# Kernel optimization log

Measured on AMD Instinct MI355X. Metric: run time of the kernel, lower is better.

The kernel has to match this reference:

```python
import jax, jax.numpy as jnp
import numpy as np

B, S, D = 16, 4096, 64
N_HASHES, BUCKET_SIZE = 8, 64
TOKEN_SELF_ATTN_VALUE = -50000.0


def setup_inputs() -> dict:
    key = jax.random.key(0)
    k1, k2, k3 = jax.random.split(key, 3)
    qk = jax.random.normal(k1, (B, S, D), jnp.float32)
    v = jax.random.normal(k2, (B, S, D), jnp.float32)
    # random rotations for LSH hashing: (batch, dim, n_hashes, n_buckets//2)
    rotations = jax.random.normal(k3, (B, D, N_HASHES, (S // BUCKET_SIZE) // 2), jnp.float32)
    return {"qk": qk, "v": v, "rotations": rotations}


def _look_one_back(x):
    # concat each chunk with the previous chunk (wrapping): (b, c, n, ...) -> (b, c, 2n, ...)
    return jnp.concatenate([x, jnp.roll(x, 1, axis=1)], axis=2)


def _lsh_attention(qk, v, rotations):
    b, s, d = qk.shape
    n_buckets = s // BUCKET_SIZE
    # --- hash vectors (rehash_each_round=True path) ---
    rotated = jnp.einsum('btf,bfhi->bhti', qk, rotations)          # (b, h, s, nb/2)
    rotated = jnp.concatenate([rotated, -rotated], axis=-1)        # (b, h, s, nb)
    buckets = jnp.argmax(rotated, axis=-1)                          # (b, h, s)
    offsets = (jnp.arange(N_HASHES) * n_buckets)[None, :, None]
    buckets = (buckets + offsets).reshape(b, -1)                    # (b, h*s)
    # --- stable bucket sort of tokens ---
    ticker = jnp.arange(N_HASHES * s)[None, :]
    buckets_and_t = s * buckets + ticker % s
    sticker = jnp.argsort(buckets_and_t, axis=-1)                   # sorted order
    undo_sort = jnp.argsort(sticker, axis=-1)
    st = sticker % s                                                # original token index
    sqk = jnp.take_along_axis(qk, st[..., None], axis=1)            # (b, h*s, d)
    sv = jnp.take_along_axis(v, st[..., None], axis=1)
    chunk_size = N_HASHES * n_buckets
    bq_t = st.reshape(b, chunk_size, -1)                            # (b, c, n)
    bqk = sqk.reshape(b, chunk_size, -1, d)                         # (b, c, n, d)
    bv = sv.reshape(b, chunk_size, -1, d)
    # shared-QK: keys are L2-normalized queries
    norm = jnp.linalg.norm(bqk, axis=-1, keepdims=True)
    bk = bqk / jnp.maximum(norm, 1e-12)
    bk = _look_one_back(bk)                                         # (b, c, 2n, d)
    bvl = _look_one_back(bv)
    bkv_t = _look_one_back(bq_t)                                    # (b, c, 2n)
    dots = jnp.einsum('bhie,bhje->bhij', bqk, bk) * (d ** -0.5)     # (b, c, n, 2n)
    # mask self-attention (token attends to itself only as last resort)
    self_mask = bq_t[:, :, :, None] == bkv_t[:, :, None, :]
    dots = jnp.where(self_mask, TOKEN_SELF_ATTN_VALUE, dots)
    # stable softmax per chunk; keep logsumexp for cross-round combination
    lse = jax.nn.logsumexp(dots, axis=-1, keepdims=True)            # (b, c, n, 1)
    p = jnp.exp(dots - lse)
    bo = jnp.einsum('buij,buje->buie', p, bvl)                      # (b, c, n, d)
    so = bo.reshape(b, -1, d)                                       # (b, h*s, d)
    slogits = lse.reshape(b, -1)                                    # (b, h*s)
    # undo the sort
    o = jnp.take_along_axis(so, undo_sort[..., None], axis=1)
    logits = jnp.take_along_axis(slogits, undo_sort, axis=1)
    o = o.reshape(b, N_HASHES, s, d)
    logits = logits.reshape(b, N_HASHES, s, 1)
    # combine hash rounds weighted by softmax over per-round logsumexp
    probs = jnp.exp(logits - jax.nn.logsumexp(logits, axis=1, keepdims=True))
    return jnp.sum(o * probs, axis=1)                               # (b, s, d)


def reference(qk, v, rotations):
    return _lsh_attention(qk, v, rotations)
```

## Files before the change

### kernel.cpp

```cpp
#include <hip/hip_runtime.h>
#include <math.h>

#define NB_B 16
#define NB_S 4096
#define NB_D 64
#define NB_H 8

#define KSTR 72
#define PSTR 136
#define VSTR 72

typedef _Float16 half_t;
typedef __attribute__((ext_vector_type(2))) _Float16 half2t;
typedef __attribute__((ext_vector_type(4))) _Float16 half4;
typedef __attribute__((ext_vector_type(8))) _Float16 half8;
typedef __attribute__((ext_vector_type(4))) float floatx4;

__global__ __launch_bounds__(256) void prep_kernel(const float* __restrict__ qk,
                                                   const float* __restrict__ v,
                                                   half_t* __restrict__ khat,
                                                   half_t* __restrict__ vh,
                                                   float* __restrict__ norm) {
  int g = blockIdx.x * 256 + threadIdx.x;
  float4 qv = ((const float4*)qk)[g];
  float4 vv = ((const float4*)v)[g];
  float ss = qv.x * qv.x + qv.y * qv.y + qv.z * qv.z + qv.w * qv.w;
  for (int off = 1; off < 16; off <<= 1) ss += __shfl_xor(ss, off);
  float nr = fmaxf(sqrtf(ss), 1e-12f);
  float sc = 1.0f / nr;
  half4 hk = {(half_t)(qv.x * sc), (half_t)(qv.y * sc), (half_t)(qv.z * sc),
              (half_t)(qv.w * sc)};
  half4 hv = {(half_t)vv.x, (half_t)vv.y, (half_t)vv.z, (half_t)vv.w};
  ((half4*)khat)[g] = hk;
  ((half4*)vh)[g] = hv;
  if ((threadIdx.x & 15) == 0) norm[g >> 4] = nr;
}

__global__ __launch_bounds__(256) void hash_kernel(const float* __restrict__ qk,
                                                   const float* __restrict__ rot,
                                                   int* __restrict__ bkt) {
  __shared__ float rotS[64 * 32];
  int tid = threadIdx.x;
  int blk = blockIdx.x;
  int tile = blk & 15, bh = blk >> 4;
  int h = bh & 7, b = bh >> 3;
  int t = (tile << 8) + tid;

  for (int i = tid; i < 2048; i += 256) {
    int f = i >> 5, ii = i & 31;
    rotS[i] = rot[(((size_t)b * 64 + f) * 8 + h) * 32 + ii];
  }
  __syncthreads();

  const float4* qrow = (const float4*)(qk + (((size_t)b << 12) + t) * 64);
  float qreg[64];
#pragma unroll
  for (int j = 0; j < 16; j++) *(float4*)(qreg + 4 * j) = qrow[j];

  float acc[32];
#pragma unroll
  for (int i = 0; i < 32; i++) acc[i] = 0.f;

#pragma unroll
  for (int f = 0; f < 64; f++) {
    float qf = qreg[f];
#pragma unroll
    for (int i4 = 0; i4 < 8; i4++) {
      float4 w = *(const float4*)(rotS + f * 32 + i4 * 4);
      acc[i4 * 4 + 0] = __fadd_rn(acc[i4 * 4 + 0], __fmul_rn(qf, w.x));
      acc[i4 * 4 + 1] = __fadd_rn(acc[i4 * 4 + 1], __fmul_rn(qf, w.y));
      acc[i4 * 4 + 2] = __fadd_rn(acc[i4 * 4 + 2], __fmul_rn(qf, w.z));
      acc[i4 * 4 + 3] = __fadd_rn(acc[i4 * 4 + 3], __fmul_rn(qf, w.w));
    }
  }

  float b1 = acc[0];
  int i1 = 0;
#pragma unroll
  for (int i = 1; i < 32; i++)
    if (acc[i] > b1) { b1 = acc[i]; i1 = i; }
#pragma unroll
  for (int i = 0; i < 32; i++) {
    float x = -acc[i];
    if (x > b1) { b1 = x; i1 = 32 + i; }
  }
  bkt[(((size_t)(b * 8 + h)) << 12) + t] = i1;
}

__global__ __launch_bounds__(256) void sort_kernel(const int* __restrict__ bkt,
                                                   int* __restrict__ st) {
  __shared__ int lb[4096];
  __shared__ int hist[4096];
  __shared__ int cumoff[64];
  int tid = threadIdx.x;
  int b = blockIdx.x >> 3, h = blockIdx.x & 7;
  const int* gb = bkt + (((size_t)(b * 8 + h)) << 12);
  for (int t = tid; t < 4096; t += 256) lb[t] = gb[t];
  for (int i = tid; i < 4096; i += 256) hist[i] = 0;
  __syncthreads();
  for (int t = tid; t < 4096; t += 256) atomicAdd(&hist[((t >> 6) << 6) | lb[t]], 1);
  __syncthreads();
  if (tid < 64) {
    int run = 0;
    for (int cc = 0; cc < 64; cc++) {
      int x = hist[(cc << 6) | tid];
      hist[(cc << 6) | tid] = run;
      run += x;
    }
    int s = run;
    for (int off = 1; off < 64; off <<= 1) {
      int u = __shfl_up(s, off);
      if (tid >= off) s += u;
    }
    cumoff[tid] = s - run;
  }
  __syncthreads();
  int lane = tid & 63;
  for (int p = 0; p < 16; p++) {
    int t = (p << 8) + tid;
    int vb = lb[t];
    unsigned long long m = 0xFFFFFFFFFFFFFFFFull;
#pragma unroll
    for (int bit = 0; bit < 6; bit++) {
      unsigned long long bl = __ballot((vb >> bit) & 1);
      m &= ((vb >> bit) & 1) ? bl : ~bl;
    }
    int rank = __popcll(m & ((1ull << lane) - 1ull));
    int cpos = cumoff[vb] + hist[((t >> 6) << 6) | vb] + rank;
    st[(((size_t)(b * 8 + h)) << 12) + cpos] = t;
  }
}

__global__ __launch_bounds__(256) void chunk_kernel(const half_t* __restrict__ khat,
                                                    const half_t* __restrict__ vh,
                                                    const float* __restrict__ norm,
                                                    const int* __restrict__ st,
                                                    half_t* __restrict__ oh,
                                                    float* __restrict__ lse) {
  __shared__ __align__(16) half_t Ks[128 * KSTR];
  __shared__ __align__(16) half_t Vt[64 * VSTR];
  __shared__ int tk[128];
  __shared__ float normS[64];
  int tid = threadIdx.x;
  int g = blockIdx.x & 511;
  int b = blockIdx.x >> 9;
  int h = g >> 6, c = g & 63;
  int gp = (g + 511) & 511;
  int hp = gp >> 6, cp = gp & 63;
  if (tid < 64) {
    tk[tid] = st[(((size_t)(b * 8 + h)) << 12) + (c << 6) + tid];
  } else if (tid < 128) {
    tk[tid] = st[(((size_t)(b * 8 + hp)) << 12) + (cp << 6) + (tid - 64)];
  }
  __syncthreads();
  if (tid < 64) normS[tid] = norm[(b << 12) + tk[tid]];
  for (int idx = tid; idx < 1024; idx += 256) {
    int row = idx >> 3, fo = idx & 7;
    half8 val = *(const half8*)(khat + (((size_t)(b << 12) + tk[row]) << 6) + fo * 8);
    *(half8*)(Ks + row * KSTR + fo * 8) = val;
  }
  {
    int kp = tid & 31, ch = tid >> 5;
    half8 r0 = *(const half8*)(vh + (((size_t)(b << 12) + tk[2 * kp]) << 6) + ch * 8);
    half8 r1 = *(const half8*)(vh + (((size_t)(b << 12) + tk[2 * kp + 1]) << 6) + ch * 8);
#pragma unroll
    for (int j = 0; j < 8; j++) {
      half2t pr = {r0[j], r1[j]};
      *(half2t*)(Vt + (ch * 8 + j) * VSTR + 2 * kp) = pr;
    }
  }
  __syncthreads();

  int lane = tid & 63, w = tid >> 6;
  int m = lane & 15, quad = lane >> 4;
  half8 afr[2];
#pragma unroll
  for (int ki = 0; ki < 2; ki++)
    afr[ki] = *(const half8*)(Ks + (w * 16 + m) * KSTR + ki * 32 + quad * 8);
  int ti[4];
  float scr[4];
#pragma unroll
  for (int r = 0; r < 4; r++) {
    int rr = w * 16 + quad * 4 + r;
    ti[r] = tk[rr];
    scr[r] = 0.125f * normS[rr];
  }

  float d[8][4];
#pragma unroll
  for (int nt = 0; nt < 8; nt++) {
    floatx4 acc = {0.f, 0.f, 0.f, 0.f};
#pragma unroll
    for (int ki = 0; ki < 2; ki++) {
      half8 bfr = *(const half8*)(Ks + (nt * 16 + m) * KSTR + ki * 32 + quad * 8);
      acc = __builtin_amdgcn_mfma_f32_16x16x32_f16(afr[ki], bfr, acc, 0, 0, 0);
    }
    int tj = tk[nt * 16 + m];
#pragma unroll
    for (int r = 0; r < 4; r++)
      d[nt][r] = (ti[r] == tj) ? -50000.0f : acc[r] * scr[r];
  }

  float mr[4], lr[4];
#pragma unroll
  for (int r = 0; r < 4; r++) {
    float mm = d[0][r];
#pragma unroll
    for (int nt = 1; nt < 8; nt++) mm = fmaxf(mm, d[nt][r]);
    for (int off = 1; off < 16; off <<= 1) mm = fmaxf(mm, __shfl_xor(mm, off));
    float ll = 0.f;
#pragma unroll
    for (int nt = 0; nt < 8; nt++) ll += __expf(d[nt][r] - mm);
    for (int off = 1; off < 16; off <<= 1) ll += __shfl_xor(ll, off);
    mr[r] = mm;
    lr[r] = ll;
    if (m == 0) lse[(((size_t)(b * 8 + h)) << 12) + ti[r]] = mm + __logf(ll);
  }
  __syncthreads();

  half_t* Ps = Ks;
#pragma unroll
  for (int nt = 0; nt < 8; nt++) {
#pragma unroll
    for (int r = 0; r < 4; r++) {
      Ps[(w * 16 + quad * 4 + r) * PSTR + nt * 16 + m] = (half_t)__expf(d[nt][r] - mr[r]);
    }
  }
  __syncthreads();

  half8 pfr[4];
#pragma unroll
  for (int kk = 0; kk < 4; kk++)
    pfr[kk] = *(const half8*)(Ps + (w * 16 + m) * PSTR + kk * 32 + quad * 8);

  floatx4 accO[4];
#pragma unroll
  for (int dt = 0; dt < 4; dt++) accO[dt] = (floatx4){0.f, 0.f, 0.f, 0.f};

#pragma unroll
  for (int dt = 0; dt < 4; dt++) {
#pragma unroll
    for (int kk = 0; kk < 2; kk++) {
      half8 bfr = *(const half8*)(Vt + (dt * 16 + m) * VSTR + kk * 32 + quad * 8);
      accO[dt] = __builtin_amdgcn_mfma_f32_16x16x32_f16(pfr[kk], bfr, accO[dt], 0, 0, 0);
    }
  }
  __syncthreads();

  {
    int kp = tid & 31, ch = tid >> 5;
    half8 r0 = *(const half8*)(vh + (((size_t)(b << 12) + tk[64 + 2 * kp]) << 6) + ch * 8);
    half8 r1 = *(const half8*)(vh + (((size_t)(b << 12) + tk[65 + 2 * kp]) << 6) + ch * 8);
#pragma unroll
    for (int j = 0; j < 8; j++) {
      half2t pr = {r0[j], r1[j]};
      *(half2t*)(Vt + (ch * 8 + j) * VSTR + 2 * kp) = pr;
    }
  }
  __syncthreads();

#pragma unroll
  for (int dt = 0; dt < 4; dt++) {
#pragma unroll
    for (int kk = 2; kk < 4; kk++) {
      half8 bfr = *(const half8*)(Vt + (dt * 16 + m) * VSTR + (kk - 2) * 32 + quad * 8);
      accO[dt] = __builtin_amdgcn_mfma_f32_16x16x32_f16(pfr[kk], bfr, accO[dt], 0, 0, 0);
    }
  }
  __syncthreads();

  half_t* Ot = Vt;
#pragma unroll
  for (int r = 0; r < 4; r++) {
    float inv = 1.0f / lr[r];
#pragma unroll
    for (int dt = 0; dt < 4; dt++) {
      Ot[(w * 16 + quad * 4 + r) * VSTR + dt * 16 + m] = (half_t)(accO[dt][r] * inv);
    }
  }
  __syncthreads();
  for (int idx = tid; idx < 512; idx += 256) {
    int row = idx >> 3, fo = idx & 7;
    half8 val = *(const half8*)(Ot + row * VSTR + fo * 8);
    *(half8*)(oh + ((((size_t)(b * 8 + h)) << 12) + tk[row]) * 64 + fo * 8) = val;
  }
}

__global__ __launch_bounds__(256) void combine_kernel(const half_t* __restrict__ oh,
                                                      const float* __restrict__ lse,
                                                      float* __restrict__ out) {
  int idx = blockIdx.x * 256 + threadIdx.x;
  int do8 = idx & 7;
  int ts = idx >> 3;
  int b = ts >> 12, t = ts & 4095;
  size_t base = ((size_t)b << 15) + t;
  float L[8];
  float m = -3.4e38f;
#pragma unroll
  for (int h = 0; h < 8; h++) {
    L[h] = lse[base + ((size_t)h << 12)];
    m = fmaxf(m, L[h]);
  }
  float s = 0.f;
#pragma unroll
  for (int h = 0; h < 8; h++) s += __expf(L[h] - m);
  float lt = m + __logf(s);
  float acc[8];
#pragma unroll
  for (int j = 0; j < 8; j++) acc[j] = 0.f;
#pragma unroll
  for (int h = 0; h < 8; h++) {
    float wgt = __expf(L[h] - lt);
    half8 o = *(const half8*)(oh + ((base + ((size_t)h << 12)) << 6) + do8 * 8);
#pragma unroll
    for (int j = 0; j < 8; j++) acc[j] += wgt * (float)o[j];
  }
  float* dst = out + ((((size_t)b << 12) + t) << 6) + do8 * 8;
  *(float4*)dst = (float4){acc[0], acc[1], acc[2], acc[3]};
  *(float4*)(dst + 4) = (float4){acc[4], acc[5], acc[6], acc[7]};
}

extern "C" void kernel_launch(void* const* d_in, const int* in_sizes, int n_in,
                              void* d_out, int out_size, void* d_ws, size_t ws_size,
                              hipStream_t stream) {
  const float* qk = (const float*)d_in[0];
  const float* v = (const float*)d_in[1];
  const float* rot = (const float*)d_in[2];
  float* out = (float*)d_out;

  int* bkt = (int*)d_ws;
  int* stp = bkt + NB_B * NB_H * NB_S;
  float* lse = (float*)(stp + NB_B * NB_H * NB_S);
  float* norm = lse + NB_B * NB_H * NB_S;
  half_t* khat = (half_t*)(norm + NB_B * NB_S);
  half_t* vh = khat + (size_t)NB_B * NB_S * NB_D;
  half_t* oh = vh + (size_t)NB_B * NB_S * NB_D;

  prep_kernel<<<NB_B * NB_S * 16 / 256, 256, 0, stream>>>(qk, v, khat, vh, norm);
  hash_kernel<<<NB_B * NB_H * 16, 256, 0, stream>>>(qk, rot, bkt);
  sort_kernel<<<NB_B * NB_H, 256, 0, stream>>>(bkt, stp);
  chunk_kernel<<<NB_B * 512, 256, 0, stream>>>(khat, vh, norm, stp, oh, lse);
  combine_kernel<<<NB_B * NB_S * 8 / 256, 256, 0, stream>>>(oh, lse, out);
}
```

Measured before the change: 214.1 us.

## Use fixed softmax max bound, packed fp32 hashing, and transposed MFMA output stores

```diff
diff --git a/kernel.cpp b/kernel.cpp
--- a/kernel.cpp
+++ b/kernel.cpp
@@ -15,6 +15,7 @@
 typedef __attribute__((ext_vector_type(4))) _Float16 half4;
 typedef __attribute__((ext_vector_type(8))) _Float16 half8;
 typedef __attribute__((ext_vector_type(4))) float floatx4;
+typedef __attribute__((ext_vector_type(2))) float f32x2;
 
 __global__ __launch_bounds__(256) void prep_kernel(const float* __restrict__ qk,
                                                    const float* __restrict__ v,
@@ -57,31 +58,35 @@
 #pragma unroll
   for (int j = 0; j < 16; j++) *(float4*)(qreg + 4 * j) = qrow[j];
 
-  float acc[32];
-#pragma unroll
-  for (int i = 0; i < 32; i++) acc[i] = 0.f;
-
-#pragma unroll
-  for (int f = 0; f < 64; f++) {
-    float qf = qreg[f];
-#pragma unroll
-    for (int i4 = 0; i4 < 8; i4++) {
-      float4 w = *(const float4*)(rotS + f * 32 + i4 * 4);
-      acc[i4 * 4 + 0] = __fadd_rn(acc[i4 * 4 + 0], __fmul_rn(qf, w.x));
-      acc[i4 * 4 + 1] = __fadd_rn(acc[i4 * 4 + 1], __fmul_rn(qf, w.y));
-      acc[i4 * 4 + 2] = __fadd_rn(acc[i4 * 4 + 2], __fmul_rn(qf, w.z));
-      acc[i4 * 4 + 3] = __fadd_rn(acc[i4 * 4 + 3], __fmul_rn(qf, w.w));
-    }
-  }
-
-  float b1 = acc[0];
+  f32x2 acc2[16];
+#pragma unroll
+  for (int i = 0; i < 16; i++) acc2[i] = (f32x2){0.f, 0.f};
+
+  {
+#pragma clang fp contract(off)
+#pragma unroll
+    for (int f = 0; f < 64; f++) {
+      float qf = qreg[f];
+      f32x2 q2 = {qf, qf};
+      const f32x2* wrow = (const f32x2*)(rotS + f * 32);
+#pragma unroll
+      for (int i2 = 0; i2 < 16; i2++) {
+        f32x2 prod = q2 * wrow[i2];
+        acc2[i2] = acc2[i2] + prod;
+      }
+    }
+  }
+
+  float b1 = acc2[0][0];
   int i1 = 0;
 #pragma unroll
-  for (int i = 1; i < 32; i++)
-    if (acc[i] > b1) { b1 = acc[i]; i1 = i; }
+  for (int i = 1; i < 32; i++) {
+    float x = acc2[i >> 1][i & 1];
+    if (x > b1) { b1 = x; i1 = i; }
+  }
 #pragma unroll
   for (int i = 0; i < 32; i++) {
-    float x = -acc[i];
+    float x = -acc2[i >> 1][i & 1];
     if (x > b1) { b1 = x; i1 = 32 + i; }
   }
   bkt[(((size_t)(b * 8 + h)) << 12) + t] = i1;
@@ -141,6 +146,7 @@
   __shared__ __align__(16) half_t Vt[64 * VSTR];
   __shared__ int tk[128];
   __shared__ float normS[64];
+  __shared__ float invS[64];
   int tid = threadIdx.x;
   int g = blockIdx.x & 511;
   int b = blockIdx.x >> 9;
@@ -186,7 +192,7 @@
     scr[r] = 0.125f * normS[rr];
   }
 
-  float d[8][4];
+  float p[8][4];
 #pragma unroll
   for (int nt = 0; nt < 8; nt++) {
     floatx4 acc = {0.f, 0.f, 0.f, 0.f};
@@ -198,23 +204,21 @@
     int tj = tk[nt * 16 + m];
 #pragma unroll
     for (int r = 0; r < 4; r++)
-      d[nt][r] = (ti[r] == tj) ? -50000.0f : acc[r] * scr[r];
-  }
-
-  float mr[4], lr[4];
+      p[nt][r] = (ti[r] == tj) ? 0.f : __expf(fmaf(acc[r], scr[r], -scr[r]));
+  }
+
+  float lr[4];
 #pragma unroll
   for (int r = 0; r < 4; r++) {
-    float mm = d[0][r];
-#pragma unroll
-    for (int nt = 1; nt < 8; nt++) mm = fmaxf(mm, d[nt][r]);
-    for (int off = 1; off < 16; off <<= 1) mm = fmaxf(mm, __shfl_xor(mm, off));
     float ll = 0.f;
 #pragma unroll
-    for (int nt = 0; nt < 8; nt++) ll += __expf(d[nt][r] - mm);
+    for (int nt = 0; nt < 8; nt++) ll += p[nt][r];
     for (int off = 1; off < 16; off <<= 1) ll += __shfl_xor(ll, off);
-    mr[r] = mm;
     lr[r] = ll;
-    if (m == 0) lse[(((size_t)(b * 8 + h)) << 12) + ti[r]] = mm + __logf(ll);
+    if (m == 0) {
+      lse[(((size_t)(b * 8 + h)) << 12) + ti[r]] = scr[r] + __logf(ll);
+      invS[w * 16 + quad * 4 + r] = 1.0f / ll;
+    }
   }
   __syncthreads();
 
@@ -223,7 +227,7 @@
   for (int nt = 0; nt < 8; nt++) {
 #pragma unroll
     for (int r = 0; r < 4; r++) {
-      Ps[(w * 16 + quad * 4 + r) * PSTR + nt * 16 + m] = (half_t)__expf(d[nt][r] - mr[r]);
+      Ps[(w * 16 + quad * 4 + r) * PSTR + nt * 16 + m] = (half_t)p[nt][r];
     }
   }
   __syncthreads();
@@ -241,8 +245,8 @@
   for (int dt = 0; dt < 4; dt++) {
 #pragma unroll
     for (int kk = 0; kk < 2; kk++) {
-      half8 bfr = *(const half8*)(Vt + (dt * 16 + m) * VSTR + kk * 32 + quad * 8);
-      accO[dt] = __builtin_amdgcn_mfma_f32_16x16x32_f16(pfr[kk], bfr, accO[dt], 0, 0, 0);
+      half8 vfr = *(const half8*)(Vt + (dt * 16 + m) * VSTR + kk * 32 + quad * 8);
+      accO[dt] = __builtin_amdgcn_mfma_f32_16x16x32_f16(vfr, pfr[kk], accO[dt], 0, 0, 0);
     }
   }
   __syncthreads();
@@ -263,26 +267,21 @@
   for (int dt = 0; dt < 4; dt++) {
 #pragma unroll
     for (int kk = 2; kk < 4; kk++) {
-      half8 bfr = *(const half8*)(Vt + (dt * 16 + m) * VSTR + (kk - 2) * 32 + quad * 8);
-      accO[dt] = __builtin_amdgcn_mfma_f32_16x16x32_f16(pfr[kk], bfr, accO[dt], 0, 0, 0);
-    }
-  }
-  __syncthreads();
-
-  half_t* Ot = Vt;
-#pragma unroll
-  for (int r = 0; r < 4; r++) {
-    float inv = 1.0f / lr[r];
+      half8 vfr = *(const half8*)(Vt + (dt * 16 + m) * VSTR + (kk - 2) * 32 + quad * 8);
+      accO[dt] = __builtin_amdgcn_mfma_f32_16x16x32_f16(vfr, pfr[kk], accO[dt], 0, 0, 0);
+    }
+  }
+
+  {
+    int tt = tk[w * 16 + m];
+    float inv = invS[w * 16 + m];
+    half_t* dst = oh + ((((size_t)(b * 8 + h)) << 12) + tt) * 64 + quad * 4;
 #pragma unroll
     for (int dt = 0; dt < 4; dt++) {
-      Ot[(w * 16 + quad * 4 + r) * VSTR + dt * 16 + m] = (half_t)(accO[dt][r] * inv);
-    }
-  }
-  __syncthreads();
-  for (int idx = tid; idx < 512; idx += 256) {
-    int row = idx >> 3, fo = idx & 7;
-    half8 val = *(const half8*)(Ot + row * VSTR + fo * 8);
-    *(half8*)(oh + ((((size_t)(b * 8 + h)) << 12) + tk[row]) * 64 + fo * 8) = val;
+      half4 ov = {(half_t)(accO[dt][0] * inv), (half_t)(accO[dt][1] * inv),
+                  (half_t)(accO[dt][2] * inv), (half_t)(accO[dt][3] * inv)};
+      *(half4*)(dst + dt * 16) = ov;
+    }
   }
 }
 
```

Result: no change. 215.0 us (+0.4%).
